# Kernel optimization log

Measured on AMD Instinct MI355X. Metric: run time of the kernel, lower is better.

The kernel has to match this reference:

```python
import jax, jax.numpy as jnp
import numpy as np

B, S, D = 4, 2048, 1024
H, HD = 16, 64
ROT_DIM = 64
ROT_BASE = 10000.0


def setup_inputs() -> dict:
    key = jax.random.key(0)
    ks = jax.random.split(key, 5)
    return {
        "hidden_states": jax.random.normal(ks[0], (B, S, D), dtype=jnp.float32),
        "Wqkv_w": jax.random.normal(ks[1], (3 * D, D), dtype=jnp.float32) * 0.02,
        "Wqkv_b": jax.random.normal(ks[2], (3 * D,), dtype=jnp.float32) * 0.02,
        "Wo_w": jax.random.normal(ks[3], (D, D), dtype=jnp.float32) * 0.02,
        "Wo_b": jax.random.normal(ks[4], (D,), dtype=jnp.float32) * 0.02,
    }


def _rope_cos_sin(seqlen, dtype):
    inv_freq = 1.0 / (ROT_BASE ** (jnp.arange(0, ROT_DIM, 2, dtype=jnp.float32) / ROT_DIM))
    t = jnp.arange(seqlen, dtype=jnp.float32)
    freqs = jnp.einsum("s,f->sf", t, inv_freq)  # (S, ROT_DIM//2)
    return jnp.cos(freqs).astype(dtype), jnp.sin(freqs).astype(dtype)


def _apply_rope(x, cos, sin):
    # x: (B, S, H, HD), non-interleaved rotary on first ROT_DIM dims
    ro, pas = x[..., :ROT_DIM], x[..., ROT_DIM:]
    x1, x2 = ro[..., : ROT_DIM // 2], ro[..., ROT_DIM // 2 :]
    c = cos[None, :, None, :]  # (1, S, 1, ROT_DIM//2)
    s = sin[None, :, None, :]
    rot = jnp.concatenate([x1 * c - x2 * s, x1 * s + x2 * c], axis=-1)
    return jnp.concatenate([rot, pas], axis=-1) if pas.shape[-1] else rot


def reference(hidden_states, Wqkv_w, Wqkv_b, Wo_w, Wo_b):
    b, s, d = hidden_states.shape
    qkv = hidden_states @ Wqkv_w.T + Wqkv_b  # (B, S, 3D)
    qkv = qkv.reshape(b, s, 3, H, HD)
    q, k, v = qkv[:, :, 0], qkv[:, :, 1], qkv[:, :, 2]  # each (B, S, H, HD)
    cos, sin = _rope_cos_sin(s, hidden_states.dtype)
    q = _apply_rope(q, cos, sin)
    k = _apply_rope(k, cos, sin)
    scale = 1.0 / jnp.sqrt(jnp.asarray(HD, hidden_states.dtype))
    scores = jnp.einsum("bqhd,bkhd->bhqk", q, k) * scale
    probs = jax.nn.softmax(scores, axis=-1)
    attn = jnp.einsum("bhqk,bkhd->bqhd", probs, v)  # (B, S, H, HD)
    attn = attn.reshape(b, s, d)
    return attn @ Wo_w.T + Wo_b
```

## Files before the change

kernel.cpp:

```cpp
#include <hip/hip_runtime.h>
#include <hip/hip_bf16.h>
#include <cstdint>
#include <cstddef>

typedef __bf16 bf16;
typedef __bf16 bf16x4 __attribute__((ext_vector_type(4)));
typedef __bf16 bf16x8 __attribute__((ext_vector_type(8)));
typedef float f32x4 __attribute__((ext_vector_type(4)));

#define NB 4
#define NS 2048
#define ND 1024
#define NH 16
#define NHD 64
#define NM (NB * NS)

#define QSCALE 0.18033688011112042f

__device__ inline void lds_dma16(const bf16* g, bf16* l) {
    __builtin_amdgcn_global_load_lds(
        (const __attribute__((address_space(1))) void*)g,
        (__attribute__((address_space(3))) void*)l, 16, 0, 0);
}

#define NHS4 2097152
#define NWQ4 786432
__global__ void prep_kernel(const float4* __restrict__ hs, const float4* __restrict__ wq,
                            float* __restrict__ cost, float* __restrict__ sint,
                            bf16x4* __restrict__ X, bf16x4* __restrict__ Wb) {
    int i = blockIdx.x * 256 + threadIdx.x;
    if (i < NS * 32) {
        int s = i >> 5, f = i & 31;
        float inv = exp2f(-(float)f * (13.287712379549449f / 32.0f));
        float ang = (float)s * inv;
        cost[i] = cosf(ang);
        sint[i] = sinf(ang);
    }
    if (i < NHS4) {
        float4 v = hs[i];
        bf16x4 r = {(bf16)v.x, (bf16)v.y, (bf16)v.z, (bf16)v.w};
        X[i] = r;
    } else {
        int j = i - NHS4;
        float4 v = wq[j];
        bf16x4 r = {(bf16)v.x, (bf16)v.y, (bf16)v.z, (bf16)v.w};
        Wb[j] = r;
    }
}

__global__ void cvt_bf16_kernel(const float4* __restrict__ in, bf16x4* __restrict__ out) {
    int i = blockIdx.x * 256 + threadIdx.x;
    float4 v = in[i];
    bf16x4 r = {(bf16)v.x, (bf16)v.y, (bf16)v.z, (bf16)v.w};
    out[i] = r;
}

__global__ void __launch_bounds__(256) qkv_rope_gemm(
    const bf16* __restrict__ A, const bf16* __restrict__ W,
    const float* __restrict__ bias,
    const float* __restrict__ cost, const float* __restrict__ sint,
    bf16* __restrict__ Qw, bf16* __restrict__ Kw, bf16* __restrict__ Vt) {
    __shared__ __attribute__((aligned(16))) bf16 lA[128 * 32];
    __shared__ __attribute__((aligned(16))) bf16 lB[128 * 32];

    int t = threadIdx.x, lane = t & 63, w = t >> 6;
    int col = lane & 15, quad = lane >> 4;
    int m0 = blockIdx.y * 128, n0 = blockIdx.x * 128;
    int wm = (w >> 1) * 64, wn = (w & 1) * 64;

    f32x4 acc[4][4];
#pragma unroll
    for (int i = 0; i < 4; ++i)
#pragma unroll
        for (int j = 0; j < 4; ++j) acc[i][j] = (f32x4){0.f, 0.f, 0.f, 0.f};

    const bf16* gA0 = A + (size_t)(m0 + w * 32 + (lane >> 2)) * ND + (lane & 3) * 8;
    const bf16* gA1 = gA0 + (size_t)16 * ND;
    const bf16* gB0 = W + (size_t)(n0 + w * 32 + (lane >> 2)) * ND + (lane & 3) * 8;
    const bf16* gB1 = gB0 + (size_t)16 * ND;
    bf16* ldsA0 = &lA[(w * 32) * 32];
    bf16* ldsA1 = &lA[(w * 32 + 16) * 32];
    bf16* ldsB0 = &lB[(w * 32) * 32];
    bf16* ldsB1 = &lB[(w * 32 + 16) * 32];

    for (int kt = 0; kt < ND; kt += 32) {
        lds_dma16(gA0 + kt, ldsA0);
        lds_dma16(gA1 + kt, ldsA1);
        lds_dma16(gB0 + kt, ldsB0);
        lds_dma16(gB1 + kt, ldsB1);
        __syncthreads();
        bf16x8 af[4], bg[4];
#pragma unroll
        for (int i = 0; i < 4; ++i)
            af[i] = *(const bf16x8*)&lA[(wm + i * 16 + col) * 32 + quad * 8];
#pragma unroll
        for (int j = 0; j < 4; ++j)
            bg[j] = *(const bf16x8*)&lB[(wn + j * 16 + col) * 32 + quad * 8];
#pragma unroll
        for (int i = 0; i < 4; ++i)
#pragma unroll
            for (int j = 0; j < 4; ++j)
                acc[i][j] = __builtin_amdgcn_mfma_f32_16x16x32_bf16(af[i], bg[j], acc[i][j], 0, 0, 0);
        __syncthreads();
    }

    int nseg = n0 + wn;
    int which = nseg >> 10;
    int h = (nseg >> 6) & (NH - 1);
    float bj[4];
#pragma unroll
    for (int j = 0; j < 4; ++j) bj[j] = bias[nseg + j * 16 + col];

    if (which == 2) {
        int mbase = m0 + wm;
        int b = mbase >> 11;
        bf16* dsth = Vt + (size_t)(b * NH + h) * NHD * NS;
#pragma unroll
        for (int i = 0; i < 4; ++i) {
            int s = ((mbase + i * 16) & (NS - 1)) + quad * 4;
#pragma unroll
            for (int j = 0; j < 4; ++j) {
                bf16x4 pv = {(bf16)(acc[i][j][0] + bj[j]), (bf16)(acc[i][j][1] + bj[j]),
                             (bf16)(acc[i][j][2] + bj[j]), (bf16)(acc[i][j][3] + bj[j])};
                *(bf16x4*)(dsth + (size_t)(j * 16 + col) * NS + s) = pv;
            }
        }
    } else {
        float sc = which ? 1.0f : QSCALE;
#pragma unroll
        for (int i = 0; i < 4; ++i) {
#pragma unroll
            for (int r = 0; r < 4; ++r) {
                int m = m0 + wm + i * 16 + quad * 4 + r;
                int b = m >> 11, s = m & (NS - 1);
                float v0 = acc[i][0][r] + bj[0];
                float v1 = acc[i][1][r] + bj[1];
                float v2 = acc[i][2][r] + bj[2];
                float v3 = acc[i][3][r] + bj[3];
                bf16* dst = (which ? Kw : Qw) + ((size_t)(b * NH + h) * NS + s) * NHD;
                float c0 = cost[s * 32 + col], s0 = sint[s * 32 + col];
                float c1 = cost[s * 32 + 16 + col], s1 = sint[s * 32 + 16 + col];
                dst[col] = (bf16)((v0 * c0 - v2 * s0) * sc);
                dst[16 + col] = (bf16)((v1 * c1 - v3 * s1) * sc);
                dst[32 + col] = (bf16)((v0 * s0 + v2 * c0) * sc);
                dst[48 + col] = (bf16)((v1 * s1 + v3 * c1) * sc);
            }
        }
    }
}

__global__ void __launch_bounds__(256, 2) attn_kernel(
    const bf16* __restrict__ Qw, const bf16* __restrict__ Kw,
    const bf16* __restrict__ Vt, bf16* __restrict__ X) {
    const int LDK = 72;
    const int LV = 36;
    __shared__ __attribute__((aligned(16))) bf16 lK[2][32 * LDK];
    __shared__ __attribute__((aligned(16))) bf16 lV[2][64 * LV];

    int t = threadIdx.x, lane = t & 63, w = t >> 6;
    int col = lane & 15, q = lane >> 4;
    int bh = blockIdx.y, b = bh >> 4, h = bh & 15;
    int q0 = blockIdx.x * 256 + w * 64;
    const bf16* Qh = Qw + (size_t)bh * NS * NHD;
    const bf16* Kh = Kw + (size_t)bh * NS * NHD;
    const bf16* Vh = Vt + (size_t)bh * NHD * NS;

    int krow = t >> 3, kc = t & 7;
    int vrow = t >> 2, vc = t & 3;
    const bf16* gK = Kh + (size_t)krow * NHD + kc * 8;
    const bf16* gV = Vh + (size_t)vrow * NS + vc * 8;
    int wKoff = krow * LDK + kc * 8;
    int wVoff = vrow * LV + vc * 8;

    bf16x8 bQ[4][2];
#pragma unroll
    for (int mb = 0; mb < 4; ++mb)
#pragma unroll
        for (int h2 = 0; h2 < 2; ++h2)
            bQ[mb][h2] = *(const bf16x8*)(Qh + (size_t)(q0 + mb * 16 + col) * NHD + h2 * 32 + q * 8);

    f32x4 o[4][4];
#pragma unroll
    for (int mb = 0; mb < 4; ++mb)
#pragma unroll
        for (int hb = 0; hb < 4; ++hb) o[mb][hb] = (f32x4){0.f, 0.f, 0.f, 0.f};
    f32x4 dacc[4];
#pragma unroll
    for (int mb = 0; mb < 4; ++mb) dacc[mb] = (f32x4){0.f, 0.f, 0.f, 0.f};

    const bf16 one = (bf16)1.0f;
    bf16x8 ones = {one, one, one, one, one, one, one, one};

    bf16x8 kr[2], vr[2];
    kr[0] = *(const bf16x8*)gK;
    vr[0] = *(const bf16x8*)gV;
    kr[1] = *(const bf16x8*)(gK + (size_t)32 * NHD);
    vr[1] = *(const bf16x8*)(gV + 32);
    *(bf16x8*)&lK[0][wKoff] = kr[0];
    *(bf16x8*)&lV[0][wVoff] = vr[0];

#pragma unroll 2
    for (int it = 0; it < 64; ++it) {
        __syncthreads();
        int cur = it & 1, nxt = cur ^ 1;
        if (it + 2 < 64) {
            kr[cur] = *(const bf16x8*)(gK + (size_t)(it + 2) * 32 * NHD);
            vr[cur] = *(const bf16x8*)(gV + (it + 2) * 32);
        }

        bf16x8 aK[2][2];
#pragma unroll
        for (int tb = 0; tb < 2; ++tb)
#pragma unroll
            for (int h2 = 0; h2 < 2; ++h2)
                aK[tb][h2] = *(const bf16x8*)&lK[cur][(tb * 16 + col) * LDK + h2 * 32 + q * 8];
        bf16x8 vf[4];
#pragma unroll
        for (int hb = 0; hb < 4; ++hb) {
            const bf16* vp = &lV[cur][(hb * 16 + col) * LV + q * 4];
            bf16x4 lo = *(const bf16x4*)vp;
            bf16x4 hi = *(const bf16x4*)(vp + 16);
            vf[hb] = __builtin_shufflevector(lo, hi, 0, 1, 2, 3, 4, 5, 6, 7);
        }
        __builtin_amdgcn_s_setprio(1);
#pragma unroll
        for (int mb = 0; mb < 4; ++mb) {
            f32x4 s0 = (f32x4){0.f, 0.f, 0.f, 0.f};
            f32x4 s1 = (f32x4){0.f, 0.f, 0.f, 0.f};
            s0 = __builtin_amdgcn_mfma_f32_16x16x32_bf16(aK[0][0], bQ[mb][0], s0, 0, 0, 0);
            s0 = __builtin_amdgcn_mfma_f32_16x16x32_bf16(aK[0][1], bQ[mb][1], s0, 0, 0, 0);
            s1 = __builtin_amdgcn_mfma_f32_16x16x32_bf16(aK[1][0], bQ[mb][0], s1, 0, 0, 0);
            s1 = __builtin_amdgcn_mfma_f32_16x16x32_bf16(aK[1][1], bQ[mb][1], s1, 0, 0, 0);
            bf16x8 pf;
#pragma unroll
            for (int r = 0; r < 4; ++r) {
                float p0 = __builtin_amdgcn_exp2f(s0[r]);
                float p1 = __builtin_amdgcn_exp2f(s1[r]);
                pf[r] = (bf16)p0;
                pf[4 + r] = (bf16)p1;
            }
            dacc[mb] = __builtin_amdgcn_mfma_f32_16x16x32_bf16(ones, pf, dacc[mb], 0, 0, 0);
#pragma unroll
            for (int hb = 0; hb < 4; ++hb)
                o[mb][hb] = __builtin_amdgcn_mfma_f32_16x16x32_bf16(vf[hb], pf, o[mb][hb], 0, 0, 0);
        }
        __builtin_amdgcn_s_setprio(0);

        if (it + 1 < 64) {
            *(bf16x8*)&lK[nxt][wKoff] = kr[nxt];
            *(bf16x8*)&lV[nxt][wVoff] = vr[nxt];
        }
    }

#pragma unroll
    for (int mb = 0; mb < 4; ++mb) {
        float linv = 1.0f / dacc[mb][0];
        int s = q0 + mb * 16 + col;
        bf16* dst = X + (size_t)(b * NS + s) * ND + h * NHD;
#pragma unroll
        for (int hb = 0; hb < 4; ++hb) {
            bf16x4 ov = {(bf16)(o[mb][hb][0] * linv), (bf16)(o[mb][hb][1] * linv),
                         (bf16)(o[mb][hb][2] * linv), (bf16)(o[mb][hb][3] * linv)};
            *(bf16x4*)(dst + hb * 16 + q * 4) = ov;
        }
    }
}

__global__ void __launch_bounds__(256) out_gemm(
    const bf16* __restrict__ A, const bf16* __restrict__ W,
    const float* __restrict__ bias, float* __restrict__ out) {
    __shared__ __attribute__((aligned(16))) bf16 lA[128 * 32];
    __shared__ __attribute__((aligned(16))) bf16 lB[128 * 32];

    int t = threadIdx.x, lane = t & 63, w = t >> 6;
    int col = lane & 15, quad = lane >> 4;
    int m0 = blockIdx.y * 128, n0 = blockIdx.x * 128;
    int wm = (w >> 1) * 64, wn = (w & 1) * 64;

    f32x4 acc[4][4];
#pragma unroll
    for (int i = 0; i < 4; ++i)
#pragma unroll
        for (int j = 0; j < 4; ++j) acc[i][j] = (f32x4){0.f, 0.f, 0.f, 0.f};

    const bf16* gA0 = A + (size_t)(m0 + w * 32 + (lane >> 2)) * ND + (lane & 3) * 8;
    const bf16* gA1 = gA0 + (size_t)16 * ND;
    const bf16* gB0 = W + (size_t)(n0 + w * 32 + (lane >> 2)) * ND + (lane & 3) * 8;
    const bf16* gB1 = gB0 + (size_t)16 * ND;
    bf16* ldsA0 = &lA[(w * 32) * 32];
    bf16* ldsA1 = &lA[(w * 32 + 16) * 32];
    bf16* ldsB0 = &lB[(w * 32) * 32];
    bf16* ldsB1 = &lB[(w * 32 + 16) * 32];

    for (int kt = 0; kt < ND; kt += 32) {
        lds_dma16(gA0 + kt, ldsA0);
        lds_dma16(gA1 + kt, ldsA1);
        lds_dma16(gB0 + kt, ldsB0);
        lds_dma16(gB1 + kt, ldsB1);
        __syncthreads();
        bf16x8 af[4], bg[4];
#pragma unroll
        for (int i = 0; i < 4; ++i)
            af[i] = *(const bf16x8*)&lA[(wm + i * 16 + col) * 32 + quad * 8];
#pragma unroll
        for (int j = 0; j < 4; ++j)
            bg[j] = *(const bf16x8*)&lB[(wn + j * 16 + col) * 32 + quad * 8];
#pragma unroll
        for (int i = 0; i < 4; ++i)
#pragma unroll
            for (int j = 0; j < 4; ++j)
                acc[i][j] = __builtin_amdgcn_mfma_f32_16x16x32_bf16(af[i], bg[j], acc[i][j], 0, 0, 0);
        __syncthreads();
    }

    float bj[4];
#pragma unroll
    for (int j = 0; j < 4; ++j) bj[j] = bias[n0 + wn + j * 16 + col];
#pragma unroll
    for (int i = 0; i < 4; ++i)
#pragma unroll
        for (int r = 0; r < 4; ++r) {
            int m = m0 + wm + i * 16 + quad * 4 + r;
#pragma unroll
            for (int j = 0; j < 4; ++j)
                out[(size_t)m * ND + n0 + wn + j * 16 + col] = acc[i][j][r] + bj[j];
        }
}

extern "C" void kernel_launch(void* const* d_in, const int* in_sizes, int n_in,
                              void* d_out, int out_size, void* d_ws, size_t ws_size,
                              hipStream_t stream) {
    const float* hs = (const float*)d_in[0];
    const float* Wqkv = (const float*)d_in[1];
    const float* bqkv = (const float*)d_in[2];
    const float* Wo = (const float*)d_in[3];
    const float* bo = (const float*)d_in[4];
    float* out = (float*)d_out;

    char* ws = (char*)d_ws;
    float* cost = (float*)ws;
    float* sint = cost + NS * 32;
    bf16* Qw = (bf16*)(ws + 524288);
    bf16* Kw = Qw + (size_t)NB * NH * NS * NHD;
    bf16* Vt = Kw + (size_t)NB * NH * NS * NHD;
    bf16* X = Vt + (size_t)NB * NH * NS * NHD;
    bf16* Wqkv_b = (bf16*)d_out;
    bf16* Wo_b = Qw;

    prep_kernel<<<dim3((NHS4 + NWQ4) / 256), dim3(256), 0, stream>>>(
        (const float4*)hs, (const float4*)Wqkv, cost, sint, (bf16x4*)X, (bf16x4*)Wqkv_b);
    qkv_rope_gemm<<<dim3(3 * ND / 128, NM / 128), dim3(256), 0, stream>>>(
        X, Wqkv_b, bqkv, cost, sint, Qw, Kw, Vt);
    attn_kernel<<<dim3(NS / 256, NB * NH), dim3(256), 0, stream>>>(Qw, Kw, Vt, X);
    cvt_bf16_kernel<<<dim3(ND * ND / 4 / 256), dim3(256), 0, stream>>>(
        (const float4*)Wo, (bf16x4*)Wo_b);
    out_gemm<<<dim3(ND / 128, NM / 128), dim3(256), 0, stream>>>(X, Wo_b, bo, out);
}
```

Baseline: 268.1 us.

## Double-buffer GEMM LDS loads, remap block order, fold Wo conversion into prep

Both GEMM kernels now double-buffer their LDS tiles, so the global-to-LDS DMA for the next K slice is issued before the MFMAs on the current slice. Each K step then needs one barrier instead of two, and MFMA priority is raised during the compute phase. Block indices are remapped so that consecutive blocks spread across groups of 8, aiming at better cache locality across XCDs. When the workspace is large enough, the Wo float-to-bf16 conversion moves into the prep kernel, removing a separate launch. This doubles LDS use per block, which may lower occupancy.

```diff
diff --git a/kernel.cpp b/kernel.cpp
--- a/kernel.cpp
+++ b/kernel.cpp
@@ -25,9 +25,12 @@
 
 #define NHS4 2097152
 #define NWQ4 786432
+#define NWO4 262144
 __global__ void prep_kernel(const float4* __restrict__ hs, const float4* __restrict__ wq,
+                            const float4* __restrict__ wo,
                             float* __restrict__ cost, float* __restrict__ sint,
-                            bf16x4* __restrict__ X, bf16x4* __restrict__ Wb) {
+                            bf16x4* __restrict__ X, bf16x4* __restrict__ Wb,
+                            bf16x4* __restrict__ Wob) {
     int i = blockIdx.x * 256 + threadIdx.x;
     if (i < NS * 32) {
         int s = i >> 5, f = i & 31;
@@ -40,11 +43,16 @@
         float4 v = hs[i];
         bf16x4 r = {(bf16)v.x, (bf16)v.y, (bf16)v.z, (bf16)v.w};
         X[i] = r;
-    } else {
+    } else if (i < NHS4 + NWQ4) {
         int j = i - NHS4;
         float4 v = wq[j];
         bf16x4 r = {(bf16)v.x, (bf16)v.y, (bf16)v.z, (bf16)v.w};
         Wb[j] = r;
+    } else {
+        int j = i - NHS4 - NWQ4;
+        float4 v = wo[j];
+        bf16x4 r = {(bf16)v.x, (bf16)v.y, (bf16)v.z, (bf16)v.w};
+        Wob[j] = r;
     }
 }
 
@@ -60,12 +68,15 @@
     const float* __restrict__ bias,
     const float* __restrict__ cost, const float* __restrict__ sint,
     bf16* __restrict__ Qw, bf16* __restrict__ Kw, bf16* __restrict__ Vt) {
-    __shared__ __attribute__((aligned(16))) bf16 lA[128 * 32];
-    __shared__ __attribute__((aligned(16))) bf16 lB[128 * 32];
+    __shared__ __attribute__((aligned(16))) bf16 lA[2][128 * 32];
+    __shared__ __attribute__((aligned(16))) bf16 lB[2][128 * 32];
 
     int t = threadIdx.x, lane = t & 63, w = t >> 6;
     int col = lane & 15, quad = lane >> 4;
-    int m0 = blockIdx.y * 128, n0 = blockIdx.x * 128;
+    int p = blockIdx.y * 24 + blockIdx.x;
+    int L = (p & 7) * 192 + (p >> 3);
+    int bx = L % 24, by = L / 24;
+    int m0 = by * 128, n0 = bx * 128;
     int wm = (w >> 1) * 64, wn = (w & 1) * 64;
 
     f32x4 acc[4][4];
@@ -78,30 +89,47 @@
     const bf16* gA1 = gA0 + (size_t)16 * ND;
     const bf16* gB0 = W + (size_t)(n0 + w * 32 + (lane >> 2)) * ND + (lane & 3) * 8;
     const bf16* gB1 = gB0 + (size_t)16 * ND;
-    bf16* ldsA0 = &lA[(w * 32) * 32];
-    bf16* ldsA1 = &lA[(w * 32 + 16) * 32];
-    bf16* ldsB0 = &lB[(w * 32) * 32];
-    bf16* ldsB1 = &lB[(w * 32 + 16) * 32];
-
-    for (int kt = 0; kt < ND; kt += 32) {
-        lds_dma16(gA0 + kt, ldsA0);
-        lds_dma16(gA1 + kt, ldsA1);
-        lds_dma16(gB0 + kt, ldsB0);
-        lds_dma16(gB1 + kt, ldsB1);
-        __syncthreads();
+    bf16* la = &lA[0][0];
+    bf16* lb = &lB[0][0];
+    int sA0 = w * 1024, sA1 = w * 1024 + 512;
+
+    lds_dma16(gA0, la + sA0);
+    lds_dma16(gA1, la + sA1);
+    lds_dma16(gB0, lb + sA0);
+    lds_dma16(gB1, lb + sA1);
+    asm volatile("s_waitcnt vmcnt(0)" ::: "memory");
+    __builtin_amdgcn_s_barrier();
+    asm volatile("" ::: "memory");
+
+#pragma unroll 2
+    for (int kt = 0; kt < 32; ++kt) {
+        int cur = kt & 1, nb = cur ^ 1;
+        if (kt + 1 < 32) {
+            int kn = (kt + 1) * 32;
+            lds_dma16(gA0 + kn, la + nb * 4096 + sA0);
+            lds_dma16(gA1 + kn, la + nb * 4096 + sA1);
+            lds_dma16(gB0 + kn, lb + nb * 4096 + sA0);
+            lds_dma16(gB1 + kn, lb + nb * 4096 + sA1);
+        }
+        const bf16* lac = la + cur * 4096;
+        const bf16* lbc = lb + cur * 4096;
         bf16x8 af[4], bg[4];
 #pragma unroll
         for (int i = 0; i < 4; ++i)
-            af[i] = *(const bf16x8*)&lA[(wm + i * 16 + col) * 32 + quad * 8];
+            af[i] = *(const bf16x8*)&lac[(wm + i * 16 + col) * 32 + quad * 8];
 #pragma unroll
         for (int j = 0; j < 4; ++j)
-            bg[j] = *(const bf16x8*)&lB[(wn + j * 16 + col) * 32 + quad * 8];
+            bg[j] = *(const bf16x8*)&lbc[(wn + j * 16 + col) * 32 + quad * 8];
+        __builtin_amdgcn_s_setprio(1);
 #pragma unroll
         for (int i = 0; i < 4; ++i)
 #pragma unroll
             for (int j = 0; j < 4; ++j)
                 acc[i][j] = __builtin_amdgcn_mfma_f32_16x16x32_bf16(af[i], bg[j], acc[i][j], 0, 0, 0);
-        __syncthreads();
+        __builtin_amdgcn_s_setprio(0);
+        if (kt + 1 < 32) asm volatile("s_waitcnt vmcnt(0)" ::: "memory");
+        __builtin_amdgcn_s_barrier();
+        asm volatile("" ::: "memory");
     }
 
     int nseg = n0 + wn;
@@ -269,12 +297,15 @@
 __global__ void __launch_bounds__(256) out_gemm(
     const bf16* __restrict__ A, const bf16* __restrict__ W,
     const float* __restrict__ bias, float* __restrict__ out) {
-    __shared__ __attribute__((aligned(16))) bf16 lA[128 * 32];
-    __shared__ __attribute__((aligned(16))) bf16 lB[128 * 32];
+    __shared__ __attribute__((aligned(16))) bf16 lA[2][128 * 32];
+    __shared__ __attribute__((aligned(16))) bf16 lB[2][128 * 32];
 
     int t = threadIdx.x, lane = t & 63, w = t >> 6;
     int col = lane & 15, quad = lane >> 4;
-    int m0 = blockIdx.y * 128, n0 = blockIdx.x * 128;
+    int p = blockIdx.y * 8 + blockIdx.x;
+    int L = (p & 7) * 64 + (p >> 3);
+    int bx = L & 7, by = L >> 3;
+    int m0 = by * 128, n0 = bx * 128;
     int wm = (w >> 1) * 64, wn = (w & 1) * 64;
 
     f32x4 acc[4][4];
@@ -287,30 +318,47 @@
     const bf16* gA1 = gA0 + (size_t)16 * ND;
     const bf16* gB0 = W + (size_t)(n0 + w * 32 + (lane >> 2)) * ND + (lane & 3) * 8;
     const bf16* gB1 = gB0 + (size_t)16 * ND;
-    bf16* ldsA0 = &lA[(w * 32) * 32];
-    bf16* ldsA1 = &lA[(w * 32 + 16) * 32];
-    bf16* ldsB0 = &lB[(w * 32) * 32];
-    bf16* ldsB1 = &lB[(w * 32 + 16) * 32];
-
-    for (int kt = 0; kt < ND; kt += 32) {
-        lds_dma16(gA0 + kt, ldsA0);
-        lds_dma16(gA1 + kt, ldsA1);
-        lds_dma16(gB0 + kt, ldsB0);
-        lds_dma16(gB1 + kt, ldsB1);
-        __syncthreads();
+    bf16* la = &lA[0][0];
+    bf16* lb = &lB[0][0];
+    int sA0 = w * 1024, sA1 = w * 1024 + 512;
+
+    lds_dma16(gA0, la + sA0);
+    lds_dma16(gA1, la + sA1);
+    lds_dma16(gB0, lb + sA0);
+    lds_dma16(gB1, lb + sA1);
+    asm volatile("s_waitcnt vmcnt(0)" ::: "memory");
+    __builtin_amdgcn_s_barrier();
+    asm volatile("" ::: "memory");
+
+#pragma unroll 2
+    for (int kt = 0; kt < 32; ++kt) {
+        int cur = kt & 1, nb = cur ^ 1;
+        if (kt + 1 < 32) {
+            int kn = (kt + 1) * 32;
+            lds_dma16(gA0 + kn, la + nb * 4096 + sA0);
+            lds_dma16(gA1 + kn, la + nb * 4096 + sA1);
+            lds_dma16(gB0 + kn, lb + nb * 4096 + sA0);
+            lds_dma16(gB1 + kn, lb + nb * 4096 + sA1);
+        }
+        const bf16* lac = la + cur * 4096;
+        const bf16* lbc = lb + cur * 4096;
         bf16x8 af[4], bg[4];
 #pragma unroll
         for (int i = 0; i < 4; ++i)
-            af[i] = *(const bf16x8*)&lA[(wm + i * 16 + col) * 32 + quad * 8];
+            af[i] = *(const bf16x8*)&lac[(wm + i * 16 + col) * 32 + quad * 8];
 #pragma unroll
         for (int j = 0; j < 4; ++j)
-            bg[j] = *(const bf16x8*)&lB[(wn + j * 16 + col) * 32 + quad * 8];
+            bg[j] = *(const bf16x8*)&lbc[(wn + j * 16 + col) * 32 + quad * 8];
+        __builtin_amdgcn_s_setprio(1);
 #pragma unroll
         for (int i = 0; i < 4; ++i)
 #pragma unroll
             for (int j = 0; j < 4; ++j)
                 acc[i][j] = __builtin_amdgcn_mfma_f32_16x16x32_bf16(af[i], bg[j], acc[i][j], 0, 0, 0);
-        __syncthreads();
+        __builtin_amdgcn_s_setprio(0);
+        if (kt + 1 < 32) asm volatile("s_waitcnt vmcnt(0)" ::: "memory");
+        __builtin_amdgcn_s_barrier();
+        asm volatile("" ::: "memory");
     }
 
     float bj[4];
@@ -345,14 +393,20 @@
     bf16* Vt = Kw + (size_t)NB * NH * NS * NHD;
     bf16* X = Vt + (size_t)NB * NH * NS * NHD;
     bf16* Wqkv_b = (bf16*)d_out;
-    bf16* Wo_b = Qw;
-
-    prep_kernel<<<dim3((NHS4 + NWQ4) / 256), dim3(256), 0, stream>>>(
-        (const float4*)hs, (const float4*)Wqkv, cost, sint, (bf16x4*)X, (bf16x4*)Wqkv_b);
+
+    const size_t base_end = 524288 + (size_t)4 * NB * NH * NS * NHD * 2;
+    bool fuse_wo = ws_size >= base_end + (size_t)ND * ND * 2;
+    bf16* Wo_b = fuse_wo ? (bf16*)(ws + base_end) : Qw;
+
+    int prep_blocks = (NHS4 + NWQ4 + (fuse_wo ? NWO4 : 0)) / 256;
+    prep_kernel<<<dim3(prep_blocks), dim3(256), 0, stream>>>(
+        (const float4*)hs, (const float4*)Wqkv, (const float4*)Wo,
+        cost, sint, (bf16x4*)X, (bf16x4*)Wqkv_b, (bf16x4*)Wo_b);
     qkv_rope_gemm<<<dim3(3 * ND / 128, NM / 128), dim3(256), 0, stream>>>(
         X, Wqkv_b, bqkv, cost, sint, Qw, Kw, Vt);
     attn_kernel<<<dim3(NS / 256, NB * NH), dim3(256), 0, stream>>>(Qw, Kw, Vt, X);
-    cvt_bf16_kernel<<<dim3(ND * ND / 4 / 256), dim3(256), 0, stream>>>(
-        (const float4*)Wo, (bf16x4*)Wo_b);
+    if (!fuse_wo)
+        cvt_bf16_kernel<<<dim3(ND * ND / 4 / 256), dim3(256), 0, stream>>>(
+            (const float4*)Wo, (bf16x4*)Wo_b);
     out_gemm<<<dim3(ND / 128, NM / 128), dim3(256), 0, stream>>>(X, Wo_b, bo, out);
 }
```

New measurement: 265.5 us. No clear change (-1.0%).

## Use K=64 tiles with XOR-swizzled LDS in GEMMs and fold Wo conversion into prep

Applied to the files above, without the earlier changes.

Both projection GEMMs now stage 64-wide K slices instead of 32. Each thread issues four cooperative DMA loads per matrix into an XOR-swizzled shared-memory layout, which halves the number of barrier pairs and is meant to avoid LDS bank conflicts on fragment reads. When the workspace is large enough, the Wo float-to-bf16 conversion is merged into the prep kernel, which removes one launch. LDS use per block doubles, which may lower occupancy.

```diff
diff --git a/kernel.cpp b/kernel.cpp
--- a/kernel.cpp
+++ b/kernel.cpp
@@ -25,9 +25,12 @@
 
 #define NHS4 2097152
 #define NWQ4 786432
+#define NWO4 262144
 __global__ void prep_kernel(const float4* __restrict__ hs, const float4* __restrict__ wq,
+                            const float4* __restrict__ wo,
                             float* __restrict__ cost, float* __restrict__ sint,
-                            bf16x4* __restrict__ X, bf16x4* __restrict__ Wb) {
+                            bf16x4* __restrict__ X, bf16x4* __restrict__ Wb,
+                            bf16x4* __restrict__ Wob) {
     int i = blockIdx.x * 256 + threadIdx.x;
     if (i < NS * 32) {
         int s = i >> 5, f = i & 31;
@@ -40,11 +43,16 @@
         float4 v = hs[i];
         bf16x4 r = {(bf16)v.x, (bf16)v.y, (bf16)v.z, (bf16)v.w};
         X[i] = r;
-    } else {
+    } else if (i < NHS4 + NWQ4) {
         int j = i - NHS4;
         float4 v = wq[j];
         bf16x4 r = {(bf16)v.x, (bf16)v.y, (bf16)v.z, (bf16)v.w};
         Wb[j] = r;
+    } else {
+        int j = i - NHS4 - NWQ4;
+        float4 v = wo[j];
+        bf16x4 r = {(bf16)v.x, (bf16)v.y, (bf16)v.z, (bf16)v.w};
+        Wob[j] = r;
     }
 }
 
@@ -60,8 +68,8 @@
     const float* __restrict__ bias,
     const float* __restrict__ cost, const float* __restrict__ sint,
     bf16* __restrict__ Qw, bf16* __restrict__ Kw, bf16* __restrict__ Vt) {
-    __shared__ __attribute__((aligned(16))) bf16 lA[128 * 32];
-    __shared__ __attribute__((aligned(16))) bf16 lB[128 * 32];
+    __shared__ __attribute__((aligned(16))) bf16 lA[128 * 64];
+    __shared__ __attribute__((aligned(16))) bf16 lB[128 * 64];
 
     int t = threadIdx.x, lane = t & 63, w = t >> 6;
     int col = lane & 15, quad = lane >> 4;
@@ -74,33 +82,38 @@
 #pragma unroll
         for (int j = 0; j < 4; ++j) acc[i][j] = (f32x4){0.f, 0.f, 0.f, 0.f};
 
-    const bf16* gA0 = A + (size_t)(m0 + w * 32 + (lane >> 2)) * ND + (lane & 3) * 8;
-    const bf16* gA1 = gA0 + (size_t)16 * ND;
-    const bf16* gB0 = W + (size_t)(n0 + w * 32 + (lane >> 2)) * ND + (lane & 3) * 8;
-    const bf16* gB1 = gB0 + (size_t)16 * ND;
-    bf16* ldsA0 = &lA[(w * 32) * 32];
-    bf16* ldsA1 = &lA[(w * 32 + 16) * 32];
-    bf16* ldsB0 = &lB[(w * 32) * 32];
-    bf16* ldsB1 = &lB[(w * 32 + 16) * 32];
-
-    for (int kt = 0; kt < ND; kt += 32) {
-        lds_dma16(gA0 + kt, ldsA0);
-        lds_dma16(gA1 + kt, ldsA1);
-        lds_dma16(gB0 + kt, ldsB0);
-        lds_dma16(gB1 + kt, ldsB1);
-        __syncthreads();
-        bf16x8 af[4], bg[4];
-#pragma unroll
-        for (int i = 0; i < 4; ++i)
-            af[i] = *(const bf16x8*)&lA[(wm + i * 16 + col) * 32 + quad * 8];
-#pragma unroll
-        for (int j = 0; j < 4; ++j)
-            bg[j] = *(const bf16x8*)&lB[(wn + j * 16 + col) * 32 + quad * 8];
-#pragma unroll
-        for (int i = 0; i < 4; ++i)
+    int srow = t >> 3;
+    int sslot = (t & 7) ^ (srow & 7);
+    const bf16* gA = A + (size_t)(m0 + srow) * ND + sslot * 8;
+    const bf16* gB = W + (size_t)(n0 + srow) * ND + sslot * 8;
+
+    int aRow = (wm + col) * 64;
+    int bRow = (wn + col) * 64;
+
+    for (int kt = 0; kt < 16; ++kt) {
+        int kc = kt * 64;
+#pragma unroll
+        for (int c = 0; c < 4; ++c) {
+            lds_dma16(gA + (size_t)(c * 32) * ND + kc, &lA[c * 2048 + t * 8]);
+            lds_dma16(gB + (size_t)(c * 32) * ND + kc, &lB[c * 2048 + t * 8]);
+        }
+        __syncthreads();
+#pragma unroll
+        for (int kh = 0; kh < 2; ++kh) {
+            int sk = ((kh * 4 + quad) ^ (col & 7)) * 8;
+            bf16x8 af[4], bg[4];
+#pragma unroll
+            for (int i = 0; i < 4; ++i)
+                af[i] = *(const bf16x8*)&lA[aRow + i * 1024 + sk];
 #pragma unroll
             for (int j = 0; j < 4; ++j)
-                acc[i][j] = __builtin_amdgcn_mfma_f32_16x16x32_bf16(af[i], bg[j], acc[i][j], 0, 0, 0);
+                bg[j] = *(const bf16x8*)&lB[bRow + j * 1024 + sk];
+#pragma unroll
+            for (int i = 0; i < 4; ++i)
+#pragma unroll
+                for (int j = 0; j < 4; ++j)
+                    acc[i][j] = __builtin_amdgcn_mfma_f32_16x16x32_bf16(af[i], bg[j], acc[i][j], 0, 0, 0);
+        }
         __syncthreads();
     }
 
@@ -269,8 +282,8 @@
 __global__ void __launch_bounds__(256) out_gemm(
     const bf16* __restrict__ A, const bf16* __restrict__ W,
     const float* __restrict__ bias, float* __restrict__ out) {
-    __shared__ __attribute__((aligned(16))) bf16 lA[128 * 32];
-    __shared__ __attribute__((aligned(16))) bf16 lB[128 * 32];
+    __shared__ __attribute__((aligned(16))) bf16 lA[128 * 64];
+    __shared__ __attribute__((aligned(16))) bf16 lB[128 * 64];
 
     int t = threadIdx.x, lane = t & 63, w = t >> 6;
     int col = lane & 15, quad = lane >> 4;
@@ -283,33 +296,37 @@
 #pragma unroll
         for (int j = 0; j < 4; ++j) acc[i][j] = (f32x4){0.f, 0.f, 0.f, 0.f};
 
-    const bf16* gA0 = A + (size_t)(m0 + w * 32 + (lane >> 2)) * ND + (lane & 3) * 8;
-    const bf16* gA1 = gA0 + (size_t)16 * ND;
-    const bf16* gB0 = W + (size_t)(n0 + w * 32 + (lane >> 2)) * ND + (lane & 3) * 8;
-    const bf16* gB1 = gB0 + (size_t)16 * ND;
-    bf16* ldsA0 = &lA[(w * 32) * 32];
-    bf16* ldsA1 = &lA[(w * 32 + 16) * 32];
-    bf16* ldsB0 = &lB[(w * 32) * 32];
-    bf16* ldsB1 = &lB[(w * 32 + 16) * 32];
-
-    for (int kt = 0; kt < ND; kt += 32) {
-        lds_dma16(gA0 + kt, ldsA0);
-        lds_dma16(gA1 + kt, ldsA1);
-        lds_dma16(gB0 + kt, ldsB0);
-        lds_dma16(gB1 + kt, ldsB1);
-        __syncthreads();
-        bf16x8 af[4], bg[4];
-#pragma unroll
-        for (int i = 0; i < 4; ++i)
-            af[i] = *(const bf16x8*)&lA[(wm + i * 16 + col) * 32 + quad * 8];
-#pragma unroll
-        for (int j = 0; j < 4; ++j)
-            bg[j] = *(const bf16x8*)&lB[(wn + j * 16 + col) * 32 + quad * 8];
-#pragma unroll
-        for (int i = 0; i < 4; ++i)
+    int srow = t >> 3;
+    int sslot = (t & 7) ^ (srow & 7);
+    const bf16* gA = A + (size_t)(m0 + srow) * ND + sslot * 8;
+    const bf16* gB = W + (size_t)(n0 + srow) * ND + sslot * 8;
+    int aRow = (wm + col) * 64;
+    int bRow = (wn + col) * 64;
+
+    for (int kt = 0; kt < 16; ++kt) {
+        int kc = kt * 64;
+#pragma unroll
+        for (int c = 0; c < 4; ++c) {
+            lds_dma16(gA + (size_t)(c * 32) * ND + kc, &lA[c * 2048 + t * 8]);
+            lds_dma16(gB + (size_t)(c * 32) * ND + kc, &lB[c * 2048 + t * 8]);
+        }
+        __syncthreads();
+#pragma unroll
+        for (int kh = 0; kh < 2; ++kh) {
+            int sk = ((kh * 4 + quad) ^ (col & 7)) * 8;
+            bf16x8 af[4], bg[4];
+#pragma unroll
+            for (int i = 0; i < 4; ++i)
+                af[i] = *(const bf16x8*)&lA[aRow + i * 1024 + sk];
 #pragma unroll
             for (int j = 0; j < 4; ++j)
-                acc[i][j] = __builtin_amdgcn_mfma_f32_16x16x32_bf16(af[i], bg[j], acc[i][j], 0, 0, 0);
+                bg[j] = *(const bf16x8*)&lB[bRow + j * 1024 + sk];
+#pragma unroll
+            for (int i = 0; i < 4; ++i)
+#pragma unroll
+                for (int j = 0; j < 4; ++j)
+                    acc[i][j] = __builtin_amdgcn_mfma_f32_16x16x32_bf16(af[i], bg[j], acc[i][j], 0, 0, 0);
+        }
         __syncthreads();
     }
 
@@ -345,14 +362,20 @@
     bf16* Vt = Kw + (size_t)NB * NH * NS * NHD;
     bf16* X = Vt + (size_t)NB * NH * NS * NHD;
     bf16* Wqkv_b = (bf16*)d_out;
-    bf16* Wo_b = Qw;
-
-    prep_kernel<<<dim3((NHS4 + NWQ4) / 256), dim3(256), 0, stream>>>(
-        (const float4*)hs, (const float4*)Wqkv, cost, sint, (bf16x4*)X, (bf16x4*)Wqkv_b);
+
+    const size_t base_end = 524288 + (size_t)4 * NB * NH * NS * NHD * 2;
+    bool fuse_wo = ws_size >= base_end + (size_t)ND * ND * 2;
+    bf16* Wo_b = fuse_wo ? (bf16*)(ws + base_end) : Qw;
+
+    int prep_blocks = (NHS4 + NWQ4 + (fuse_wo ? NWO4 : 0)) / 256;
+    prep_kernel<<<dim3(prep_blocks), dim3(256), 0, stream>>>(
+        (const float4*)hs, (const float4*)Wqkv, (const float4*)Wo,
+        cost, sint, (bf16x4*)X, (bf16x4*)Wqkv_b, (bf16x4*)Wo_b);
     qkv_rope_gemm<<<dim3(3 * ND / 128, NM / 128), dim3(256), 0, stream>>>(
         X, Wqkv_b, bqkv, cost, sint, Qw, Kw, Vt);
     attn_kernel<<<dim3(NS / 256, NB * NH), dim3(256), 0, stream>>>(Qw, Kw, Vt, X);
-    cvt_bf16_kernel<<<dim3(ND * ND / 4 / 256), dim3(256), 0, stream>>>(
-        (const float4*)Wo, (bf16x4*)Wo_b);
+    if (!fuse_wo)
+        cvt_bf16_kernel<<<dim3(ND * ND / 4 / 256), dim3(256), 0, stream>>>(
+            (const float4*)Wo, (bf16x4*)Wo_b);
     out_gemm<<<dim3(ND / 128, NM / 128), dim3(256), 0, stream>>>(X, Wo_b, bo, out);
 }
```

New measurement: 256.9 us, median of 2. 1.04x faster.
